# Performance work log

Hardware: AMD Instinct MI355X
Metric: run time of the kernel (lower is better)

Reference implementation:

```python
import jax, jax.numpy as jnp
import numpy as np

Z_DIM = 128
E_L_STEPS = 60
E_L_STEP_SIZE = 0.4
E_ALPHA = 1.0
E_BETA = 1.0
E_GAMMA = 1.0
E_PRIOR_SIG = 1.0
E_L_WITH_NOISE = True
BATCH = 65536


def _linear_init(k, fin, fout):
    # torch nn.Linear default: U(-1/sqrt(fin), 1/sqrt(fin)) for weight and bias
    s = 1.0 / np.sqrt(fin)
    kw, kb = jax.random.split(k)
    W = jax.random.uniform(kw, (fin, fout), minval=-s, maxval=s, dtype=jnp.float32)
    b = jax.random.uniform(kb, (fout,), minval=-s, maxval=s, dtype=jnp.float32)
    return W, b


def setup_inputs() -> dict:
    key = jax.random.key(0)
    k1, k2, k3, kz = jax.random.split(key, 4)
    W1, b1 = _linear_init(k1, Z_DIM, 512)
    W2, b2 = _linear_init(k2, 512, 64)
    W3, b3 = _linear_init(k3, 64, 1)
    z = jax.random.normal(kz, (BATCH, Z_DIM), dtype=jnp.float32)
    return {"z": z, "W1": W1, "b1": b1, "W2": W2, "b2": b2, "W3": W3, "b3": b3}


def _energy_sum(z, W1, b1, W2, b2, W3, b3):
    # NetE: Linear(z_dim,512) -> GELU -> Linear(512,64) -> GELU -> Linear(64,1)
    h = jax.nn.gelu(z @ W1 + b1, approximate=False)
    h = jax.nn.gelu(h @ W2 + b2, approximate=False)
    return jnp.sum(h @ W3 + b3)


def reference(z, W1, b1, W2, b2, W3, b3):
    noise_key = jax.random.key(42)
    coef_grad = -E_ALPHA * 0.5 * E_L_STEP_SIZE * E_L_STEP_SIZE
    coef_prior = -E_BETA * 0.5 * E_L_STEP_SIZE * E_L_STEP_SIZE / (E_PRIOR_SIG * E_PRIOR_SIG)
    grad_fn = jax.grad(lambda zz: _energy_sum(zz, W1, b1, W2, b2, W3, b3))

    def step(zz, i):
        g = grad_fn(zz)  # dE/dz, shape [B, z_dim]
        upd = coef_grad * g + coef_prior * zz
        if E_L_WITH_NOISE:
            noise = jax.random.normal(jax.random.fold_in(noise_key, i), zz.shape, zz.dtype)
            upd = upd + E_GAMMA * E_L_STEP_SIZE * noise
        return zz + upd, None

    z_final, _ = jax.lax.scan(step, z, jnp.arange(E_L_STEPS))
    return z_final
```

## Files before the change

kernel.cpp:

```cpp
#include <hip/hip_runtime.h>
#include <stdint.h>


#define BATCH   65536
#define ZDIM    128
#define H1      512
#define H2      64
#define NSTEP   60
#define COEF    (-0.08f)

using bf16x8 = __attribute__((ext_vector_type(8))) short;
using f32x4  = __attribute__((ext_vector_type(4))) float;

#define MFMA16(a, b, c) __builtin_amdgcn_mfma_f32_16x16x32_bf16((a), (b), (c), 0, 0, 0)

__device__ __forceinline__ uint32_t rotl32(uint32_t v, int s) {
  return (v << s) | (v >> (32 - s));
}

__device__ __forceinline__ void tf2x32(uint32_t k0, uint32_t k1,
                                       uint32_t x0, uint32_t x1,
                                       uint32_t& o0, uint32_t& o1) {
  const uint32_t k2 = k0 ^ k1 ^ 0x1BD11BDAu;
  x0 += k0; x1 += k1;
  x0 += x1; x1 = rotl32(x1, 13); x1 ^= x0;
  x0 += x1; x1 = rotl32(x1, 15); x1 ^= x0;
  x0 += x1; x1 = rotl32(x1, 26); x1 ^= x0;
  x0 += x1; x1 = rotl32(x1,  6); x1 ^= x0;
  x0 += k1; x1 += k2 + 1u;
  x0 += x1; x1 = rotl32(x1, 17); x1 ^= x0;
  x0 += x1; x1 = rotl32(x1, 29); x1 ^= x0;
  x0 += x1; x1 = rotl32(x1, 16); x1 ^= x0;
  x0 += x1; x1 = rotl32(x1, 24); x1 ^= x0;
  x0 += k2; x1 += k0 + 2u;
  x0 += x1; x1 = rotl32(x1, 13); x1 ^= x0;
  x0 += x1; x1 = rotl32(x1, 15); x1 ^= x0;
  x0 += x1; x1 = rotl32(x1, 26); x1 ^= x0;
  x0 += x1; x1 = rotl32(x1,  6); x1 ^= x0;
  x0 += k0; x1 += k1 + 3u;
  x0 += x1; x1 = rotl32(x1, 17); x1 ^= x0;
  x0 += x1; x1 = rotl32(x1, 29); x1 ^= x0;
  x0 += x1; x1 = rotl32(x1, 16); x1 ^= x0;
  x0 += x1; x1 = rotl32(x1, 24); x1 ^= x0;
  x0 += k1; x1 += k2 + 4u;
  x0 += x1; x1 = rotl32(x1, 13); x1 ^= x0;
  x0 += x1; x1 = rotl32(x1, 15); x1 ^= x0;
  x0 += x1; x1 = rotl32(x1, 26); x1 ^= x0;
  x0 += x1; x1 = rotl32(x1,  6); x1 ^= x0;
  x0 += k2; x1 += k0 + 5u;
  o0 = x0; o1 = x1;
}

__device__ __forceinline__ float normal_from_bits(uint32_t bits) {
  float u01 = __uint_as_float((bits >> 9) | 0x3F800000u) - 1.0f;
  const float lo = -0.99999994f;
  float u = fmaxf(lo, u01 * 2.0f + lo);
  float w = -__logf(fmaf(-u, u, 1.0f));
  float p;
  if (w < 5.0f) {
    w -= 2.5f;
    p =             2.81022636e-08f;
    p = fmaf(p, w,  3.43273939e-07f);
    p = fmaf(p, w, -3.5233877e-06f);
    p = fmaf(p, w, -4.39150654e-06f);
    p = fmaf(p, w,  0.00021858087f);
    p = fmaf(p, w, -0.00125372503f);
    p = fmaf(p, w, -0.00417768164f);
    p = fmaf(p, w,  0.246640727f);
    p = fmaf(p, w,  1.50140941f);
  } else {
    w = sqrtf(w) - 3.0f;
    p =            -0.000200214257f;
    p = fmaf(p, w,  0.000100950558f);
    p = fmaf(p, w,  0.00134934322f);
    p = fmaf(p, w, -0.00367342844f);
    p = fmaf(p, w,  0.00573950773f);
    p = fmaf(p, w, -0.0076224613f);
    p = fmaf(p, w,  0.00943887047f);
    p = fmaf(p, w,  1.00167406f);
    p = fmaf(p, w,  2.83297682f);
  }
  return 1.41421356f * (p * u);
}

struct N4 { float v[4]; };
__device__ __forceinline__ N4 noise4(uint32_t k0, uint32_t k1, uint32_t f0) {
  const uint32_t k2 = k0 ^ k1 ^ 0x1BD11BDAu;
  uint32_t x0[4], x1[4];
  #pragma unroll
  for (int i = 0; i < 4; ++i) { x0[i] = k0; x1[i] = (f0 + 128u * (uint32_t)i) + k1; }
#define TFG(ra, rb, rc, rd, ia, ib, ic)                                        \
  _Pragma("unroll")                                                            \
  for (int i = 0; i < 4; ++i) {                                                \
    x0[i] += x1[i]; x1[i] = rotl32(x1[i], ra); x1[i] ^= x0[i];                 \
    x0[i] += x1[i]; x1[i] = rotl32(x1[i], rb); x1[i] ^= x0[i];                 \
    x0[i] += x1[i]; x1[i] = rotl32(x1[i], rc); x1[i] ^= x0[i];                 \
    x0[i] += x1[i]; x1[i] = rotl32(x1[i], rd); x1[i] ^= x0[i];                 \
    x0[i] += (ia); x1[i] += (ib) + (ic); }
  TFG(13, 15, 26,  6, k1, k2, 1u)
  TFG(17, 29, 16, 24, k2, k0, 2u)
  TFG(13, 15, 26,  6, k0, k1, 3u)
  TFG(17, 29, 16, 24, k1, k2, 4u)
  TFG(13, 15, 26,  6, k2, k0, 5u)
#undef TFG
  N4 r;
  #pragma unroll
  for (int i = 0; i < 4; ++i) r.v[i] = normal_from_bits(x0[i] ^ x1[i]);
  return r;
}

__device__ __forceinline__ float sigm(float y) {
  return __fdividef(1.0f, 1.0f + __expf(-y));
}
__device__ __forceinline__ float gelu_fast(float x) { return x * sigm(1.702f * x); }
__device__ __forceinline__ float gelu_grad_fast(float x) {
  float s = sigm(1.702f * x);
  return fmaf(1.702f * x, s * (1.0f - s), s);
}

__device__ __forceinline__ float gelu_exact(float x) {
  return 0.5f * x * (1.0f + erff(x * 0.70710678f));
}
__device__ __forceinline__ float gelu_grad_exact(float x) {
  float u   = x * 0.70710678f;
  float cdf = 0.5f * (1.0f + erff(u));
  float pdf = 0.39894228040143267f * expf(-u * u);
  return fmaf(x, pdf, cdf);
}

__device__ __forceinline__ unsigned short f2bf(float x) {
  return (unsigned short)(__float_as_uint(x) >> 16);
}

__global__ void pack_b(const float* __restrict__ src, unsigned short* __restrict__ dst,
                       int K, int N, int trans, int total, float scale) {
  int o = blockIdx.x * 256 + threadIdx.x;
  if (o >= total) return;
  int t   = o >> 9;
  int rem = o & 511;
  int l = rem >> 3, j = rem & 7;
  int nb = N >> 4;
  int kb = t / nb, cb = t - kb * nb;
  int k = kb * 32 + (l >> 4) * 8 + j;
  int n = cb * 16 + (l & 15);
  float v = trans ? src[(size_t)n * K + k] : src[(size_t)k * N + n];
  dst[o] = f2bf(scale * v);
}

__device__ __forceinline__ bf16x8 lds_frag(const unsigned short* lds, int row,
                                           int ebase, int rowElems) {
  int e = ebase ^ ((row & 7) << 3);
  return *(const bf16x8*)(lds + row * rowElems + e);
}
__device__ __forceinline__ bf16x8 load_frag(const unsigned short* p, int tile, int lane) {
  return *(const bf16x8*)(p + tile * 512 + lane * 8);
}

__global__ __launch_bounds__(512, 4) void langevin_mfma(
    const float* __restrict__ z0,
    const float* __restrict__ b1,
    const float* __restrict__ b2,
    const float* __restrict__ W3,
    const unsigned short* __restrict__ W1p,
    const unsigned short* __restrict__ W2p,
    const unsigned short* __restrict__ W2Tp,
    const unsigned short* __restrict__ W1Tp,
    float* __restrict__ out)
{
  __shared__ unsigned short Zlds[64 * 128];
  __shared__ unsigned short HEu[64 * 64];
  __shared__ unsigned short D2lds[64 * 64];
  __shared__ float b1lds[512];
  __shared__ float b2lds[64];
  __shared__ float w3lds[64];

  const int tid  = threadIdx.x;
  const int lane = tid & 63;
  const int wid  = tid >> 6;
  const int rg   = wid >> 1;
  const int ch   = wid & 1;
  const int wg   = blockIdx.x;

  b1lds[tid] = b1[tid];
  if (tid < 64) { b2lds[tid] = b2[tid]; w3lds[tid] = W3[tid]; }

  const int rbase = rg * 16 + ((lane >> 4) << 2);
  const int clane = lane & 15;
  const int arow  = rg * 16 + clane;
  const int ahi   = (lane >> 4) << 3;

  f32x4 zacc[4];
  #pragma unroll
  for (int tl = 0; tl < 4; ++tl) {
    const int t = ch * 4 + tl;
    #pragma unroll
    for (int i = 0; i < 4; ++i) {
      int row = rbase + i;
      int col = t * 16 + clane;
      float zv = z0[(size_t)(wg * 64 + row) * ZDIM + col];
      zacc[tl][i] = zv;
      Zlds[row * 128 + (col ^ ((row & 7) << 3))] = f2bf(zv);
    }
  }

  for (int step = 0; step < NSTEP; ++step) {
    uint32_t fk0, fk1;
    tf2x32(0u, 42u, 0u, (uint32_t)step, fk0, fk1);

    f32x4 a2acc[2];
    #pragma unroll
    for (int ctl = 0; ctl < 2; ++ctl) {
      float bb = b2lds[(ch * 2 + ctl) * 16 + clane];
      a2acc[ctl] = f32x4{bb, bb, bb, bb};
    }

    #pragma unroll 1
    for (int jb = 0; jb < 8; ++jb) {
      __syncthreads();
      #pragma unroll
      for (int ctl = 0; ctl < 2; ++ctl) {
        const int ct = ch * 2 + ctl;
        f32x4 acc = f32x4{0.f, 0.f, 0.f, 0.f};
        #pragma unroll
        for (int kb = 0; kb < 4; ++kb) {
          bf16x8 za = lds_frag(Zlds, arow, kb * 32 + ahi, 128);
          acc = MFMA16(za, load_frag(W1p, kb * 32 + jb * 4 + ct, lane), acc);
        }
        float bb = b1lds[jb * 64 + ct * 16 + clane];
        #pragma unroll
        for (int i = 0; i < 4; ++i) {
          int row = rbase + i;
          int c   = ct * 16 + clane;
          HEu[row * 64 + (c ^ ((row & 7) << 3))] = f2bf(gelu_fast(acc[i] + bb));
        }
      }
      __syncthreads();
      #pragma unroll
      for (int kb = 0; kb < 2; ++kb) {
        bf16x8 ha = lds_frag(HEu, arow, kb * 32 + ahi, 64);
        #pragma unroll
        for (int ctl = 0; ctl < 2; ++ctl)
          a2acc[ctl] = MFMA16(ha, load_frag(W2p, (jb * 2 + kb) * 4 + ch * 2 + ctl, lane),
                              a2acc[ctl]);
      }
    }

    #pragma unroll
    for (int ctl = 0; ctl < 2; ++ctl) {
      const int ct = ch * 2 + ctl;
      float w3v = w3lds[ct * 16 + clane];
      #pragma unroll
      for (int i = 0; i < 4; ++i) {
        int row = rbase + i;
        int c   = ct * 16 + clane;
        D2lds[row * 64 + (c ^ ((row & 7) << 3))] = f2bf(w3v * gelu_grad_fast(a2acc[ctl][i]));
      }
    }

    {
      const uint32_t gs0 = (uint32_t)(wg * 64 + rbase) * 128u;
      #pragma unroll
      for (int tl = 0; tl < 4; ++tl) {
        N4 nz = noise4(fk0, fk1, gs0 + (uint32_t)((ch * 4 + tl) * 16 + clane));
        #pragma unroll
        for (int i = 0; i < 4; ++i) {
          float zv = zacc[tl][i];
          zacc[tl][i] = fmaf(0.4f, nz.v[i], fmaf(COEF, zv, zv));
        }
        __builtin_amdgcn_sched_barrier(0);
      }
    }

    #pragma unroll 1
    for (int jb = 0; jb < 8; ++jb) {
      __syncthreads();
      bf16x8 d2a0 = lds_frag(D2lds, arow, 0  + ahi, 64);
      bf16x8 d2a1 = lds_frag(D2lds, arow, 32 + ahi, 64);
      #pragma unroll
      for (int ctl = 0; ctl < 2; ++ctl) {
        const int ct = ch * 2 + ctl;
        f32x4 eacc = f32x4{0.f, 0.f, 0.f, 0.f};
        eacc = MFMA16(d2a0, load_frag(W2Tp,      jb * 4 + ct, lane), eacc);
        eacc = MFMA16(d2a1, load_frag(W2Tp, 32 + jb * 4 + ct, lane), eacc);
        f32x4 a1acc = f32x4{0.f, 0.f, 0.f, 0.f};
        #pragma unroll
        for (int kb = 0; kb < 4; ++kb) {
          bf16x8 za = lds_frag(Zlds, arow, kb * 32 + ahi, 128);
          a1acc = MFMA16(za, load_frag(W1p, kb * 32 + jb * 4 + ct, lane), a1acc);
        }
        float bb = b1lds[jb * 64 + ct * 16 + clane];
        #pragma unroll
        for (int i = 0; i < 4; ++i) {
          int row = rbase + i;
          int c   = ct * 16 + clane;
          float ev = eacc[i] * gelu_grad_fast(a1acc[i] + bb);
          HEu[row * 64 + (c ^ ((row & 7) << 3))] = f2bf(ev);
        }
      }
      __syncthreads();
      #pragma unroll
      for (int kb = 0; kb < 2; ++kb) {
        bf16x8 ea = lds_frag(HEu, arow, kb * 32 + ahi, 64);
        #pragma unroll
        for (int tl = 0; tl < 4; ++tl)
          zacc[tl] = MFMA16(ea, load_frag(W1Tp, (jb * 2 + kb) * 8 + ch * 4 + tl, lane),
                            zacc[tl]);
      }
    }

    #pragma unroll
    for (int tl = 0; tl < 4; ++tl) {
      const int t = ch * 4 + tl;
      #pragma unroll
      for (int i = 0; i < 4; ++i) {
        int row = rbase + i;
        int col = t * 16 + clane;
        Zlds[row * 128 + (col ^ ((row & 7) << 3))] = f2bf(zacc[tl][i]);
      }
    }
  }

  #pragma unroll
  for (int tl = 0; tl < 4; ++tl) {
    const int t = ch * 4 + tl;
    #pragma unroll
    for (int i = 0; i < 4; ++i) {
      int row = rbase + i;
      out[(size_t)(wg * 64 + row) * ZDIM + t * 16 + clane] = zacc[tl][i];
    }
  }
}

__global__ void transpose_w1(const float* __restrict__ W1, float* __restrict__ W1T) {
  int o = blockIdx.x * 256 + threadIdx.x;
  int j = o >> 7, k = o & 127;
  W1T[o] = W1[k * H1 + j];
}

__device__ __forceinline__ float normal_from_bits_exact(uint32_t bits) {
  float u01 = __uint_as_float((bits >> 9) | 0x3F800000u) - 1.0f;
  const float lo = -0.99999994f;
  float u = fmaxf(lo, u01 * 2.0f + lo);
  float w = -log1pf(-u * u);
  float p;
  if (w < 5.0f) {
    w -= 2.5f;
    p =             2.81022636e-08f;
    p = fmaf(p, w,  3.43273939e-07f);
    p = fmaf(p, w, -3.5233877e-06f);
    p = fmaf(p, w, -4.39150654e-06f);
    p = fmaf(p, w,  0.00021858087f);
    p = fmaf(p, w, -0.00125372503f);
    p = fmaf(p, w, -0.00417768164f);
    p = fmaf(p, w,  0.246640727f);
    p = fmaf(p, w,  1.50140941f);
  } else {
    w = sqrtf(w) - 3.0f;
    p =            -0.000200214257f;
    p = fmaf(p, w,  0.000100950558f);
    p = fmaf(p, w,  0.00134934322f);
    p = fmaf(p, w, -0.00367342844f);
    p = fmaf(p, w,  0.00573950773f);
    p = fmaf(p, w, -0.0076224613f);
    p = fmaf(p, w,  0.00943887047f);
    p = fmaf(p, w,  1.00167406f);
    p = fmaf(p, w,  2.83297682f);
  }
  return 1.41421356f * (p * u);
}

__global__ __launch_bounds__(256, 1) void langevin_scalar(
    const float* __restrict__ z0, const float* __restrict__ b1,
    const float* __restrict__ W2, const float* __restrict__ b2,
    const float* __restrict__ W3, const float* __restrict__ W1T,
    float* __restrict__ out)
{
  __shared__ float nbuf[256 * 33];
  const int tid = threadIdx.x;
  const uint32_t b = (uint32_t)blockIdx.x * 256u + (uint32_t)tid;
  float z[ZDIM];
  #pragma unroll
  for (int k = 0; k < ZDIM; ++k) z[k] = z0[(size_t)b * ZDIM + k];
  for (int step = 0; step < NSTEP; ++step) {
    uint32_t fk0, fk1;
    tf2x32(0u, 42u, 0u, (uint32_t)step, fk0, fk1);
    float acc2[H2];
    #pragma unroll
    for (int c = 0; c < H2; ++c) acc2[c] = b2[c];
    #pragma unroll 2
    for (int j = 0; j < H1; ++j) {
      const float* __restrict__ w = W1T + j * ZDIM;
      float s0 = 0.f, s1 = 0.f, s2 = 0.f, s3 = 0.f;
      #pragma unroll
      for (int k = 0; k < ZDIM; k += 4) {
        s0 = fmaf(z[k + 0], w[k + 0], s0); s1 = fmaf(z[k + 1], w[k + 1], s1);
        s2 = fmaf(z[k + 2], w[k + 2], s2); s3 = fmaf(z[k + 3], w[k + 3], s3);
      }
      float a1 = b1[j] + ((s0 + s1) + (s2 + s3));
      float h  = gelu_exact(a1);
      const float* __restrict__ w2r = W2 + j * H2;
      #pragma unroll
      for (int c = 0; c < H2; ++c) acc2[c] = fmaf(h, w2r[c], acc2[c]);
    }
    #pragma unroll
    for (int c = 0; c < H2; ++c) acc2[c] = W3[c] * gelu_grad_exact(acc2[c]);
    float g[ZDIM];
    #pragma unroll
    for (int k = 0; k < ZDIM; ++k) g[k] = 0.f;
    for (int j = 0; j < H1; ++j) {
      const float* __restrict__ w = W1T + j * ZDIM;
      float s0 = 0.f, s1 = 0.f, s2 = 0.f, s3 = 0.f;
      #pragma unroll
      for (int k = 0; k < ZDIM; k += 4) {
        s0 = fmaf(z[k + 0], w[k + 0], s0); s1 = fmaf(z[k + 1], w[k + 1], s1);
        s2 = fmaf(z[k + 2], w[k + 2], s2); s3 = fmaf(z[k + 3], w[k + 3], s3);
      }
      float a1 = b1[j] + ((s0 + s1) + (s2 + s3));
      const float* __restrict__ w2r = W2 + j * H2;
      float d0 = 0.f, d1 = 0.f, d2 = 0.f, d3 = 0.f;
      #pragma unroll
      for (int c = 0; c < H2; c += 4) {
        d0 = fmaf(acc2[c + 0], w2r[c + 0], d0); d1 = fmaf(acc2[c + 1], w2r[c + 1], d1);
        d2 = fmaf(acc2[c + 2], w2r[c + 2], d2); d3 = fmaf(acc2[c + 3], w2r[c + 3], d3);
      }
      float eps = ((d0 + d1) + (d2 + d3)) * gelu_grad_exact(a1);
      #pragma unroll
      for (int k = 0; k < ZDIM; ++k) g[k] = fmaf(eps, w[k], g[k]);
    }
    const uint32_t base = b * (uint32_t)ZDIM;
    #pragma unroll
    for (int kc = 0; kc < 4; ++kc) {
      for (int kk = 0; kk < 32; ++kk) {
        uint32_t f = base + (uint32_t)(kc * 32 + kk);
        uint32_t r0, r1;
        tf2x32(fk0, fk1, 0u, f, r0, r1);
        nbuf[tid * 33 + kk] = normal_from_bits_exact(r0 ^ r1);
      }
      #pragma unroll
      for (int i = 0; i < 32; ++i) {
        const int k = kc * 32 + i;
        z[k] += COEF * g[k] + COEF * z[k] + 0.4f * nbuf[tid * 33 + i];
      }
    }
  }
  #pragma unroll
  for (int k = 0; k < ZDIM; ++k) out[(size_t)b * ZDIM + k] = z[k];
}

extern "C" void kernel_launch(void* const* d_in, const int* in_sizes, int n_in,
                              void* d_out, int out_size, void* d_ws, size_t ws_size,
                              hipStream_t stream) {
  (void)in_sizes; (void)n_in; (void)out_size;

  const float* z0 = (const float*)d_in[0];
  const float* W1 = (const float*)d_in[1];
  const float* b1 = (const float*)d_in[2];
  const float* W2 = (const float*)d_in[3];
  const float* b2 = (const float*)d_in[4];
  const float* W3 = (const float*)d_in[5];
  float* out = (float*)d_out;

  const size_t NEED = 196608u * 2u;
  if (ws_size >= NEED) {
    unsigned short* W1p  = (unsigned short*)d_ws;
    unsigned short* W2p  = W1p  + 65536;
    unsigned short* W2Tp = W2p  + 32768;
    unsigned short* W1Tp = W2Tp + 32768;

    hipLaunchKernelGGL(pack_b, dim3(256), dim3(256), 0, stream, W1, W1p,  128, 512, 0, 65536, 1.0f);
    hipLaunchKernelGGL(pack_b, dim3(128), dim3(256), 0, stream, W2, W2p,  512,  64, 0, 32768, 1.0f);
    hipLaunchKernelGGL(pack_b, dim3(128), dim3(256), 0, stream, W2, W2Tp,  64, 512, 1, 32768, 1.0f);
    hipLaunchKernelGGL(pack_b, dim3(256), dim3(256), 0, stream, W1, W1Tp, 512, 128, 1, 65536, COEF);
    hipLaunchKernelGGL(langevin_mfma, dim3(BATCH / 64), dim3(512), 0, stream,
                       z0, b1, b2, W3, W1p, W2p, W2Tp, W1Tp, out);
  } else {
    float* W1T = (float*)d_ws;
    hipLaunchKernelGGL(transpose_w1, dim3(256), dim3(256), 0, stream, W1, W1T);
    hipLaunchKernelGGL(langevin_scalar, dim3(BATCH / 256), dim3(256), 0, stream,
                       z0, b1, W2, b2, W3, W1T, out);
  }
}
```

Baseline: 5.784 ms.

## Split each row group's columns across four waves using 1024-thread blocks

Doubles the block size to 1024 threads so each 16-row group is served by four waves instead of two. Each wave now owns one 16-column tile of the hidden layers and two tiles of z, roughly halving per-wave MFMA work and accumulator registers. The cost is more waves contending at each __syncthreads. Launch bounds of (1024, 4) may also force register spilling or limit how many blocks fit per CU.

```diff
diff --git a/kernel.cpp b/kernel.cpp
--- a/kernel.cpp
+++ b/kernel.cpp
@@ -156,7 +156,7 @@
   return *(const bf16x8*)(p + tile * 512 + lane * 8);
 }
 
-__global__ __launch_bounds__(512, 4) void langevin_mfma(
+__global__ __launch_bounds__(1024, 4) void langevin_mfma(
     const float* __restrict__ z0,
     const float* __restrict__ b1,
     const float* __restrict__ b2,
@@ -177,11 +177,11 @@
   const int tid  = threadIdx.x;
   const int lane = tid & 63;
   const int wid  = tid >> 6;
-  const int rg   = wid >> 1;
-  const int ch   = wid & 1;
+  const int rg   = wid >> 2;
+  const int cq   = wid & 3;
   const int wg   = blockIdx.x;
 
-  b1lds[tid] = b1[tid];
+  if (tid < 512) b1lds[tid] = b1[tid];
   if (tid < 64) { b2lds[tid] = b2[tid]; w3lds[tid] = W3[tid]; }
 
   const int rbase = rg * 16 + ((lane >> 4) << 2);
@@ -189,10 +189,10 @@
   const int arow  = rg * 16 + clane;
   const int ahi   = (lane >> 4) << 3;
 
-  f32x4 zacc[4];
-  #pragma unroll
-  for (int tl = 0; tl < 4; ++tl) {
-    const int t = ch * 4 + tl;
+  f32x4 zacc[2];
+  #pragma unroll
+  for (int tl = 0; tl < 2; ++tl) {
+    const int t = cq * 2 + tl;
     #pragma unroll
     for (int i = 0; i < 4; ++i) {
       int row = rbase + i;
@@ -207,30 +207,27 @@
     uint32_t fk0, fk1;
     tf2x32(0u, 42u, 0u, (uint32_t)step, fk0, fk1);
 
-    f32x4 a2acc[2];
-    #pragma unroll
-    for (int ctl = 0; ctl < 2; ++ctl) {
-      float bb = b2lds[(ch * 2 + ctl) * 16 + clane];
-      a2acc[ctl] = f32x4{bb, bb, bb, bb};
+    f32x4 a2acc;
+    {
+      float bb = b2lds[cq * 16 + clane];
+      a2acc = f32x4{bb, bb, bb, bb};
     }
 
     #pragma unroll 1
     for (int jb = 0; jb < 8; ++jb) {
       __syncthreads();
-      #pragma unroll
-      for (int ctl = 0; ctl < 2; ++ctl) {
-        const int ct = ch * 2 + ctl;
+      {
         f32x4 acc = f32x4{0.f, 0.f, 0.f, 0.f};
         #pragma unroll
         for (int kb = 0; kb < 4; ++kb) {
           bf16x8 za = lds_frag(Zlds, arow, kb * 32 + ahi, 128);
-          acc = MFMA16(za, load_frag(W1p, kb * 32 + jb * 4 + ct, lane), acc);
+          acc = MFMA16(za, load_frag(W1p, kb * 32 + jb * 4 + cq, lane), acc);
         }
-        float bb = b1lds[jb * 64 + ct * 16 + clane];
+        float bb = b1lds[jb * 64 + cq * 16 + clane];
         #pragma unroll
         for (int i = 0; i < 4; ++i) {
           int row = rbase + i;
-          int c   = ct * 16 + clane;
+          int c   = cq * 16 + clane;
           HEu[row * 64 + (c ^ ((row & 7) << 3))] = f2bf(gelu_fast(acc[i] + bb));
         }
       }
@@ -238,30 +235,25 @@
       #pragma unroll
       for (int kb = 0; kb < 2; ++kb) {
         bf16x8 ha = lds_frag(HEu, arow, kb * 32 + ahi, 64);
-        #pragma unroll
-        for (int ctl = 0; ctl < 2; ++ctl)
-          a2acc[ctl] = MFMA16(ha, load_frag(W2p, (jb * 2 + kb) * 4 + ch * 2 + ctl, lane),
-                              a2acc[ctl]);
-      }
-    }
-
-    #pragma unroll
-    for (int ctl = 0; ctl < 2; ++ctl) {
-      const int ct = ch * 2 + ctl;
-      float w3v = w3lds[ct * 16 + clane];
+        a2acc = MFMA16(ha, load_frag(W2p, (jb * 2 + kb) * 4 + cq, lane), a2acc);
+      }
+    }
+
+    {
+      float w3v = w3lds[cq * 16 + clane];
       #pragma unroll
       for (int i = 0; i < 4; ++i) {
         int row = rbase + i;
-        int c   = ct * 16 + clane;
-        D2lds[row * 64 + (c ^ ((row & 7) << 3))] = f2bf(w3v * gelu_grad_fast(a2acc[ctl][i]));
+        int c   = cq * 16 + clane;
+        D2lds[row * 64 + (c ^ ((row & 7) << 3))] = f2bf(w3v * gelu_grad_fast(a2acc[i]));
       }
     }
 
     {
       const uint32_t gs0 = (uint32_t)(wg * 64 + rbase) * 128u;
       #pragma unroll
-      for (int tl = 0; tl < 4; ++tl) {
-        N4 nz = noise4(fk0, fk1, gs0 + (uint32_t)((ch * 4 + tl) * 16 + clane));
+      for (int tl = 0; tl < 2; ++tl) {
+        N4 nz = noise4(fk0, fk1, gs0 + (uint32_t)((cq * 2 + tl) * 16 + clane));
         #pragma unroll
         for (int i = 0; i < 4; ++i) {
           float zv = zacc[tl][i];
@@ -276,23 +268,21 @@
       __syncthreads();
       bf16x8 d2a0 = lds_frag(D2lds, arow, 0  + ahi, 64);
       bf16x8 d2a1 = lds_frag(D2lds, arow, 32 + ahi, 64);
-      #pragma unroll
-      for (int ctl = 0; ctl < 2; ++ctl) {
-        const int ct = ch * 2 + ctl;
+      {
         f32x4 eacc = f32x4{0.f, 0.f, 0.f, 0.f};
-        eacc = MFMA16(d2a0, load_frag(W2Tp,      jb * 4 + ct, lane), eacc);
-        eacc = MFMA16(d2a1, load_frag(W2Tp, 32 + jb * 4 + ct, lane), eacc);
+        eacc = MFMA16(d2a0, load_frag(W2Tp,      jb * 4 + cq, lane), eacc);
+        eacc = MFMA16(d2a1, load_frag(W2Tp, 32 + jb * 4 + cq, lane), eacc);
         f32x4 a1acc = f32x4{0.f, 0.f, 0.f, 0.f};
         #pragma unroll
         for (int kb = 0; kb < 4; ++kb) {
           bf16x8 za = lds_frag(Zlds, arow, kb * 32 + ahi, 128);
-          a1acc = MFMA16(za, load_frag(W1p, kb * 32 + jb * 4 + ct, lane), a1acc);
+          a1acc = MFMA16(za, load_frag(W1p, kb * 32 + jb * 4 + cq, lane), a1acc);
         }
-        float bb = b1lds[jb * 64 + ct * 16 + clane];
+        float bb = b1lds[jb * 64 + cq * 16 + clane];
         #pragma unroll
         for (int i = 0; i < 4; ++i) {
           int row = rbase + i;
-          int c   = ct * 16 + clane;
+          int c   = cq * 16 + clane;
           float ev = eacc[i] * gelu_grad_fast(a1acc[i] + bb);
           HEu[row * 64 + (c ^ ((row & 7) << 3))] = f2bf(ev);
         }
@@ -302,15 +292,15 @@
       for (int kb = 0; kb < 2; ++kb) {
         bf16x8 ea = lds_frag(HEu, arow, kb * 32 + ahi, 64);
         #pragma unroll
-        for (int tl = 0; tl < 4; ++tl)
-          zacc[tl] = MFMA16(ea, load_frag(W1Tp, (jb * 2 + kb) * 8 + ch * 4 + tl, lane),
+        for (int tl = 0; tl < 2; ++tl)
+          zacc[tl] = MFMA16(ea, load_frag(W1Tp, (jb * 2 + kb) * 8 + cq * 2 + tl, lane),
                             zacc[tl]);
       }
     }
 
     #pragma unroll
-    for (int tl = 0; tl < 4; ++tl) {
-      const int t = ch * 4 + tl;
+    for (int tl = 0; tl < 2; ++tl) {
+      const int t = cq * 2 + tl;
       #pragma unroll
       for (int i = 0; i < 4; ++i) {
         int row = rbase + i;
@@ -321,8 +311,8 @@
   }
 
   #pragma unroll
-  for (int tl = 0; tl < 4; ++tl) {
-    const int t = ch * 4 + tl;
+  for (int tl = 0; tl < 2; ++tl) {
+    const int t = cq * 2 + tl;
     #pragma unroll
     for (int i = 0; i < 4; ++i) {
       int row = rbase + i;
@@ -471,7 +461,7 @@
     hipLaunchKernelGGL(pack_b, dim3(128), dim3(256), 0, stream, W2, W2p,  512,  64, 0, 32768, 1.0f);
     hipLaunchKernelGGL(pack_b, dim3(128), dim3(256), 0, stream, W2, W2Tp,  64, 512, 1, 32768, 1.0f);
     hipLaunchKernelGGL(pack_b, dim3(256), dim3(256), 0, stream, W1, W1Tp, 512, 128, 1, 65536, COEF);
-    hipLaunchKernelGGL(langevin_mfma, dim3(BATCH / 64), dim3(512), 0, stream,
+    hipLaunchKernelGGL(langevin_mfma, dim3(BATCH / 64), dim3(1024), 0, stream,
                        z0, b1, b2, W3, W1p, W2p, W2Tp, W1Tp, out);
   } else {
     float* W1T = (float*)d_ws;
```

Result: slower. 7.061 ms (+22.1%).
